# Optimization experiments

Hardware: AMD Instinct MI355X
Metric: run time of the kernel (lower is better)

## Reference

```python
import jax, jax.numpy as jnp
import numpy as np

R = 0.2          # stable-distribution hash bucket width
TABLE_SIZE = 2   # hash table size (buckets)
M = 5            # number of appended ALSH transform dims
EPS = 1e-12


def conv2d(x, W, b, pad):
    out = jax.lax.conv_general_dilated(
        x, W, window_strides=(1, 1), padding=[(pad, pad), (pad, pad)],
        dimension_numbers=('NCHW', 'OIHW', 'NCHW'))
    return out + b[None, :, None, None]


def maxpool2(x):
    return jax.lax.reduce_window(x, -jnp.inf, jax.lax.max,
                                 (1, 1, 2, 2), (1, 1, 2, 2), 'VALID')


def alsh_mask(x, W, a, c):
    """ALSH filter selection: hash P(kernels) and Q(query) with a stable
    distribution hash h(v)=floor((a.v+b)/r) mod table_size; active filters
    are those landing in the query's bucket. Returns [B, Cout] 0/1 mask.
    Multiplying conv output by this mask == gather active filters then
    zero_fill_missing back to full channel count."""
    Cout, Cin, kH, kW = W.shape
    Kf = W.reshape(Cout, -1)                       # [Cout, Cin*kH*kW]
    norms = jnp.linalg.norm(Kf, axis=1)
    Kn = Kf / (jnp.max(norms) + EPS)               # scale so all norms <= 1
    n = jnp.linalg.norm(Kn, axis=1, keepdims=True)
    # P transform: append norm^2, norm^4, ..., norm^(2^M)
    powers = jnp.concatenate([n ** (2 ** (i + 1)) for i in range(M)], axis=1)
    P = jnp.concatenate([Kn, powers], axis=1)      # [Cout, d+M]
    kh = jnp.mod(jnp.floor((P @ a + c[0]) / R), TABLE_SIZE)  # [Cout]
    # query vector: per-sample channel means broadcast over kernel support
    cm = x.mean(axis=(2, 3))                       # [B, Cin]
    q = jnp.repeat(cm, kH * kW, axis=1)            # [B, Cin*kH*kW] (cin,kh,kw order)
    qn = q / (jnp.linalg.norm(q, axis=1, keepdims=True) + EPS)
    # Q transform: append M halves
    Qv = jnp.concatenate([qn, jnp.full((q.shape[0], M), 0.5, q.dtype)], axis=1)
    qh = jnp.mod(jnp.floor((Qv @ a + c[0]) / R), TABLE_SIZE)  # [B]
    return (kh[None, :] == qh[:, None]).astype(x.dtype)       # [B, Cout]


def setup_inputs() -> dict:
    key = jax.random.key(0)
    ks = jax.random.split(key, 16)
    u = lambda k, s: jax.random.uniform(k, s, jnp.float32, 0.0, R)
    n = lambda k, s, sc=0.1: jax.random.normal(k, s, jnp.float32) * sc
    return {
        'x': jax.random.normal(ks[0], (4096, 3, 32, 32), jnp.float32),
        'W1': n(ks[1], (16, 3, 5, 5)), 'b1': n(ks[2], (16,)),
        'a1': jax.random.normal(ks[3], (80,), jnp.float32), 'c1': u(ks[4], (1,)),
        'W2': n(ks[5], (20, 16, 5, 5)), 'b2': n(ks[6], (20,)),
        'a2': jax.random.normal(ks[7], (405,), jnp.float32), 'c2': u(ks[8], (1,)),
        'W3': n(ks[9], (20, 20, 5, 5)), 'b3': n(ks[10], (20,)),
        'a3': jax.random.normal(ks[11], (505,), jnp.float32), 'c3': u(ks[12], (1,)),
        'Wo': n(ks[13], (10, 320)), 'bo': n(ks[14], (10,)),
    }


def reference(x, W1, b1, a1, c1, W2, b2, a2, c2, W3, b3, a3, c3, Wo, bo):
    m1 = alsh_mask(x, W1, a1, c1)
    h = jax.nn.relu(conv2d(x, W1, b1, 2)) * m1[:, :, None, None]
    h = maxpool2(h)                                # [B,16,16,16]
    m2 = alsh_mask(h, W2, a2, c2)
    h = jax.nn.relu(conv2d(h, W2, b2, 2)) * m2[:, :, None, None]
    h = maxpool2(h)                                # [B,20,8,8]
    m3 = alsh_mask(h, W3, a3, c3)
    h = jax.nn.relu(conv2d(h, W3, b3, 2)) * m3[:, :, None, None]
    # zero_fill_missing -> identity here: inactive channels already zero
    h = maxpool2(h)                                # [B,20,4,4]
    flat = h.reshape(h.shape[0], -1)               # [B,320]
    return flat @ Wo.T + bo
```

## Files before the change

### kernel.cpp

```cpp
#include <hip/hip_runtime.h>
#include <hip/hip_bf16.h>

#define EPSV 1e-12
#define RHASH 0.2

__device__ __forceinline__ int fmod2(double t) {
    return (int)(((long long)floor(t)) & 1LL);
}

__device__ __forceinline__ void load_row6(const float* base, float* r) {
    float2 a0 = *(const float2*)(base);
    float2 a1 = *(const float2*)(base + 2);
    float2 a2 = *(const float2*)(base + 4);
    r[0] = a0.x; r[1] = a0.y; r[2] = a1.x; r[3] = a1.y; r[4] = a2.x; r[5] = a2.y;
}

__device__ void layer_setup(const float* W, const float* a, double cval,
                            int Co, int Ci, int* kh, double* asum, double* qc,
                            double* s_norm, float* Wbuf, float* abuf)
{
    const int t = threadIdx.x;
    const int D = Ci * 25;
    for (int i = t; i < Co * D; i += 256) Wbuf[i] = W[i];
    for (int i = t; i < D + 5; i += 256) abuf[i] = a[i];
    __syncthreads();
    if (t < Co) {
        double s = 0;
        for (int j = 0; j < D; ++j) { double w = (double)Wbuf[t * D + j]; s += w * w; }
        s_norm[t] = sqrt(s);
    }
    __syncthreads();
    if (t == 0) {
        double mx = 0;
        for (int i = 0; i < Co; ++i) mx = fmax(mx, s_norm[i]);
        s_norm[23] = 1.0 / (mx + EPSV);
    }
    __syncthreads();
    double scale = s_norm[23];
    if (t < Co) {
        double dp = 0;
        for (int j = 0; j < D; ++j) dp += (double)Wbuf[t * D + j] * (double)abuf[j];
        dp *= scale;
        double n = s_norm[t] * scale;
        double p = n * n;
        for (int m = 0; m < 5; ++m) { dp += p * (double)abuf[D + m]; p *= p; }
        kh[t] = fmod2((dp + cval) / RHASH);
    }
    if (t >= 64 && t < 64 + Ci) {
        int c = t - 64;
        double s = 0;
        for (int j = 0; j < 25; ++j) s += (double)abuf[c * 25 + j];
        asum[c] = s;
    }
    if (t == 128) {
        double s = 0;
        for (int m = 0; m < 5; ++m) s += (double)abuf[D + m];
        *qc = 0.5 * s + cval;
    }
    __syncthreads();
}

__global__ __launch_bounds__(256) void setup_kernel(
    const float* W1, const float* a1, const float* c1,
    const float* W2, const float* a2, const float* c2,
    const float* W3, const float* a3, const float* c3,
    double* dmeta, int* imeta)
{
    __shared__ float Wbuf[10000];
    __shared__ float abuf[512];
    __shared__ double s_norm[24];
    layer_setup(W1, a1, (double)c1[0], 16, 3,  imeta + 0,  dmeta + 0,  dmeta + 39, s_norm, Wbuf, abuf);
    layer_setup(W2, a2, (double)c2[0], 20, 16, imeta + 16, dmeta + 3,  dmeta + 40, s_norm, Wbuf, abuf);
    layer_setup(W3, a3, (double)c3[0], 20, 20, imeta + 36, dmeta + 19, dmeta + 41, s_norm, Wbuf, abuf);
}

__global__ __launch_bounds__(256) void pack_kernel(const float* W1, const float* W2, const float* W3,
                                                   float* Wp1, float* Wp2, float* Wp3)
{
    int i = blockIdx.x * 256 + threadIdx.x;
    if (i < 1200) {
        int co = i & 15, r = i >> 4;
        int kx = r % 5, r2 = r / 5, ky = r2 % 5, ci = r2 / 5;
        Wp1[i] = W1[co * 75 + ci * 25 + ky * 5 + kx];
    } else if (i < 1200 + 8960) {
        int k = i - 1200;
        int j = k % 28, r = k / 28;
        int cog = r % 4, r2 = r / 4, ky = r2 % 5, ci = r2 / 5;
        Wp2[k] = (j < 25) ? W2[(cog * 5 + j / 5) * 400 + ci * 25 + ky * 5 + (j % 5)] : 0.f;
    } else if (i < 1200 + 8960 + 11200) {
        int k = i - 10160;
        int j = k % 28, r = k / 28;
        int cog = r % 4, r2 = r / 4, ky = r2 % 5, ci = r2 / 5;
        Wp3[k] = (j < 25) ? W3[(cog * 5 + j / 5) * 500 + ci * 25 + ky * 5 + (j % 5)] : 0.f;
    }
}

__global__ __launch_bounds__(256) void conv1_kernel(
    const float* __restrict__ x, const float* __restrict__ Wp1,
    const float* __restrict__ b1, const int* __restrict__ kh1,
    const double* __restrict__ dmeta, float* __restrict__ h1,
    int* __restrict__ qh2)
{
    __shared__ float xs[3][36][36];
    __shared__ float Ws[1200];
    __shared__ double s_red[3];
    __shared__ double s_ch[16][4];

    const int b = blockIdx.x, t = threadIdx.x;
    const int w = t >> 6, ln = t & 63;

    for (int i = t; i < 3 * 36 * 36; i += 256) (&xs[0][0][0])[i] = 0.f;
    for (int i = t; i < 600; i += 256) ((float2*)Ws)[i] = ((const float2*)Wp1)[i];
    __syncthreads();
    const float2* xb2 = (const float2*)(x + (size_t)b * 3072);
    for (int i = t; i < 1536; i += 256) {
        int idx = i * 2, c = idx >> 10, rem = idx & 1023;
        *(float2*)&xs[c][(rem >> 5) + 2][(rem & 31) + 2] = xb2[i];
    }
    __syncthreads();

    if (w < 3) {
        double s = 0;
        for (int j = 0; j < 16; ++j) {
            int i = ln + 64 * j;
            s += (double)xs[w][(i >> 5) + 2][(i & 31) + 2];
        }
        #pragma unroll
        for (int off = 32; off; off >>= 1) s += __shfl_xor(s, off);
        if (ln == 0) s_red[w] = s;
    }
    __syncthreads();
    double dp = 0, nn = 0;
    #pragma unroll
    for (int c = 0; c < 3; ++c) {
        double cm = s_red[c] * (1.0 / 1024.0);
        dp += cm * dmeta[c]; nn += cm * cm;
    }
    const int qh = fmod2((dp / (5.0 * sqrt(nn) + EPSV) + dmeta[39]) / RHASH);

    const int py = t >> 4, px = t & 15;
    const int y0 = 2 * py, x0 = 2 * px;

    float acc[16][4];
    #pragma unroll
    for (int c = 0; c < 16; ++c) {
        float bb = b1[c];
        acc[c][0] = bb; acc[c][1] = bb; acc[c][2] = bb; acc[c][3] = bb;
    }
    #pragma unroll
    for (int ci = 0; ci < 3; ++ci) {
        float cur[6], nxt[6];
        load_row6(&xs[ci][y0][x0], cur);
        load_row6(&xs[ci][y0 + 1][x0], nxt);
        #pragma unroll
        for (int ky = 0; ky < 5; ++ky) {
            const float* wbase = Ws + ((ci * 5 + ky) * 5) * 16;
            #pragma unroll
            for (int kx = 0; kx < 5; ++kx) {
                float wc[16];
                const float4* wp = (const float4*)(wbase + kx * 16);
                *(float4*)&wc[0]  = wp[0];
                *(float4*)&wc[4]  = wp[1];
                *(float4*)&wc[8]  = wp[2];
                *(float4*)&wc[12] = wp[3];
                #pragma unroll
                for (int c = 0; c < 16; ++c) {
                    acc[c][0] = fmaf(wc[c], cur[kx],     acc[c][0]);
                    acc[c][1] = fmaf(wc[c], cur[kx + 1], acc[c][1]);
                    acc[c][2] = fmaf(wc[c], nxt[kx],     acc[c][2]);
                    acc[c][3] = fmaf(wc[c], nxt[kx + 1], acc[c][3]);
                }
            }
            if (ky < 4) {
                #pragma unroll
                for (int j = 0; j < 6; ++j) cur[j] = nxt[j];
                load_row6(&xs[ci][y0 + ky + 2][x0], nxt);
            }
        }
    }

    float mv[16];
    float* hb = h1 + (size_t)b * 4096 + t;
    #pragma unroll
    for (int c = 0; c < 16; ++c) {
        float m = fmaxf(fmaxf(acc[c][0], acc[c][1]), fmaxf(acc[c][2], acc[c][3]));
        mv[c] = fmaxf(m, 0.f) * ((kh1[c] == qh) ? 1.f : 0.f);
        hb[c * 256] = mv[c];
    }
    #pragma unroll
    for (int c = 0; c < 16; ++c) {
        double s = (double)mv[c];
        #pragma unroll
        for (int off = 32; off; off >>= 1) s += __shfl_xor(s, off);
        if (ln == 0) s_ch[c][w] = s;
    }
    __syncthreads();
    if (t == 0) {
        double dp2 = 0, nn2 = 0;
        #pragma unroll
        for (int c = 0; c < 16; ++c) {
            double cm = (s_ch[c][0] + s_ch[c][1] + s_ch[c][2] + s_ch[c][3]) * (1.0 / 256.0);
            dp2 += cm * dmeta[3 + c]; nn2 += cm * cm;
        }
        qh2[b] = fmod2((dp2 / (5.0 * sqrt(nn2) + EPSV) + dmeta[40]) / RHASH);
    }
}

__global__ __launch_bounds__(256) void conv2_kernel(
    const float* __restrict__ h1, const float* __restrict__ Wp2,
    const float* __restrict__ b2, const int* __restrict__ kh2,
    const int* __restrict__ qh2, const double* __restrict__ dmeta,
    float* __restrict__ h2, int* __restrict__ qh3)
{
    __shared__ float xs[2][4][20][20];
    __shared__ float Ws[2240];
    __shared__ double s_ch[2][20];

    const int b0 = blockIdx.x * 2, t = threadIdx.x;
    const int cog = t >> 6, slot = t & 63;
    const int s = slot >> 5, py = (slot >> 2) & 7, pxp = slot & 3;
    const int y0 = 2 * py, x0a = 2 * pxp, x0b = 2 * pxp + 8;

    for (int i = t; i < 3200; i += 256) (&xs[0][0][0][0])[i] = 0.f;

    const int qh = qh2[b0 + s];
    float acc[5][8];
    #pragma unroll
    for (int c = 0; c < 5; ++c) {
        float bb = b2[cog * 5 + c];
        #pragma unroll
        for (int j = 0; j < 8; ++j) acc[c][j] = bb;
    }
    __syncthreads();

    for (int ch = 0; ch < 4; ++ch) {
        for (int i = t; i < 1120; i += 256)
            ((float2*)Ws)[i] = ((const float2*)(Wp2 + ch * 2240))[i];
        for (int i = t; i < 1024; i += 256) {
            int ss = i >> 9, r = i & 511, ci = r >> 7, rr = r & 127, p2 = rr * 2;
            *(float2*)&xs[ss][ci][(p2 >> 4) + 2][(p2 & 15) + 2] =
                ((const float2*)(h1 + (size_t)(b0 + ss) * 4096 + (ch * 4 + ci) * 256))[rr];
        }
        __syncthreads();

        #pragma unroll
        for (int ci = 0; ci < 4; ++ci) {
            float ca[6], na[6], cb[6], nb[6];
            load_row6(&xs[s][ci][y0][x0a], ca);
            load_row6(&xs[s][ci][y0 + 1][x0a], na);
            load_row6(&xs[s][ci][y0][x0b], cb);
            load_row6(&xs[s][ci][y0 + 1][x0b], nb);
            #pragma unroll
            for (int ky = 0; ky < 5; ++ky) {
                float wv[28];
                const float4* wp = (const float4*)&Ws[((ci * 5 + ky) * 4 + cog) * 28];
                *(float4*)&wv[0]  = wp[0];
                *(float4*)&wv[4]  = wp[1];
                *(float4*)&wv[8]  = wp[2];
                *(float4*)&wv[12] = wp[3];
                *(float4*)&wv[16] = wp[4];
                *(float4*)&wv[20] = wp[5];
                *(float4*)&wv[24] = wp[6];
                #pragma unroll
                for (int c = 0; c < 5; ++c) {
                    #pragma unroll
                    for (int kx = 0; kx < 5; ++kx) {
                        float wgt = wv[c * 5 + kx];
                        acc[c][0] = fmaf(wgt, ca[kx],     acc[c][0]);
                        acc[c][1] = fmaf(wgt, ca[kx + 1], acc[c][1]);
                        acc[c][2] = fmaf(wgt, na[kx],     acc[c][2]);
                        acc[c][3] = fmaf(wgt, na[kx + 1], acc[c][3]);
                        acc[c][4] = fmaf(wgt, cb[kx],     acc[c][4]);
                        acc[c][5] = fmaf(wgt, cb[kx + 1], acc[c][5]);
                        acc[c][6] = fmaf(wgt, nb[kx],     acc[c][6]);
                        acc[c][7] = fmaf(wgt, nb[kx + 1], acc[c][7]);
                    }
                }
                if (ky < 4) {
                    #pragma unroll
                    for (int j = 0; j < 6; ++j) { ca[j] = na[j]; cb[j] = nb[j]; }
                    load_row6(&xs[s][ci][y0 + ky + 2][x0a], na);
                    load_row6(&xs[s][ci][y0 + ky + 2][x0b], nb);
                }
            }
        }
        __syncthreads();
    }

    float* ob = h2 + (size_t)(b0 + s) * 1280 + py * 8 + pxp;
    double csum[5];
    #pragma unroll
    for (int c = 0; c < 5; ++c) {
        int co = cog * 5 + c;
        float mask = (kh2[co] == qh) ? 1.f : 0.f;
        float mA = fmaxf(fmaxf(acc[c][0], acc[c][1]), fmaxf(acc[c][2], acc[c][3]));
        float mB = fmaxf(fmaxf(acc[c][4], acc[c][5]), fmaxf(acc[c][6], acc[c][7]));
        float vA = fmaxf(mA, 0.f) * mask;
        float vB = fmaxf(mB, 0.f) * mask;
        ob[co * 64]     = vA;
        ob[co * 64 + 4] = vB;
        csum[c] = (double)vA + (double)vB;
    }
    #pragma unroll
    for (int c = 0; c < 5; ++c) {
        double sv = csum[c];
        #pragma unroll
        for (int off = 16; off; off >>= 1) sv += __shfl_xor(sv, off);
        if ((slot & 31) == 0) s_ch[s][cog * 5 + c] = sv;
    }
    __syncthreads();
    if (t < 2) {
        double dp2 = 0, nn2 = 0;
        #pragma unroll
        for (int c = 0; c < 20; ++c) {
            double cm = s_ch[t][c] * (1.0 / 64.0);
            dp2 += cm * dmeta[19 + c]; nn2 += cm * cm;
        }
        qh3[b0 + t] = fmod2((dp2 / (5.0 * sqrt(nn2) + EPSV) + dmeta[41]) / RHASH);
    }
}

__global__ __launch_bounds__(256) void conv3_kernel(
    const float* __restrict__ h2, const float* __restrict__ Wp3,
    const float* __restrict__ b3, const int* __restrict__ kh3,
    const int* __restrict__ qh3,
    const float* __restrict__ Wo, const float* __restrict__ bo,
    float* __restrict__ out, int B)
{
    __shared__ float xs[4][5][12][12];
    __shared__ float Ws[2800];
    __shared__ float flat[4][320];

    const int b0 = blockIdx.x * 4, t = threadIdx.x;
    const int s = t >> 6, q = t & 63, cog = q >> 4, pos = q & 15;
    const int py = pos >> 2, px = pos & 3;
    const int y0 = 2 * py, x0 = 2 * px;
    const int b = b0 + s;

    for (int i = t; i < 4 * 5 * 144; i += 256) (&xs[0][0][0][0])[i] = 0.f;

    const int qh = (b < B) ? qh3[b] : 0;
    float acc[5][4];
    #pragma unroll
    for (int c = 0; c < 5; ++c) {
        float bb = b3[cog * 5 + c];
        acc[c][0] = bb; acc[c][1] = bb; acc[c][2] = bb; acc[c][3] = bb;
    }
    __syncthreads();

    for (int ch = 0; ch < 4; ++ch) {
        for (int i = t; i < 1400; i += 256)
            ((float2*)Ws)[i] = ((const float2*)(Wp3 + ch * 2800))[i];
        for (int i = t; i < 640; i += 256) {
            int ss = i / 160, r = i - ss * 160, ci = r >> 5, rr = r & 31, p2 = rr * 2;
            if (b0 + ss < B)
                *(float2*)&xs[ss][ci][(p2 >> 3) + 2][(p2 & 7) + 2] =
                    ((const float2*)(h2 + (size_t)(b0 + ss) * 1280 + (ch * 5 + ci) * 64))[rr];
        }
        __syncthreads();

        #pragma unroll
        for (int ci = 0; ci < 5; ++ci) {
            float cur[6], nxt[6];
            load_row6(&xs[s][ci][y0][x0], cur);
            load_row6(&xs[s][ci][y0 + 1][x0], nxt);
            #pragma unroll
            for (int ky = 0; ky < 5; ++ky) {
                float wv[28];
                const float4* wp = (const float4*)&Ws[((ci * 5 + ky) * 4 + cog) * 28];
                *(float4*)&wv[0]  = wp[0];
                *(float4*)&wv[4]  = wp[1];
                *(float4*)&wv[8]  = wp[2];
                *(float4*)&wv[12] = wp[3];
                *(float4*)&wv[16] = wp[4];
                *(float4*)&wv[20] = wp[5];
                *(float4*)&wv[24] = wp[6];
                #pragma unroll
                for (int c = 0; c < 5; ++c) {
                    #pragma unroll
                    for (int kx = 0; kx < 5; ++kx) {
                        float wgt = wv[c * 5 + kx];
                        acc[c][0] = fmaf(wgt, cur[kx],     acc[c][0]);
                        acc[c][1] = fmaf(wgt, cur[kx + 1], acc[c][1]);
                        acc[c][2] = fmaf(wgt, nxt[kx],     acc[c][2]);
                        acc[c][3] = fmaf(wgt, nxt[kx + 1], acc[c][3]);
                    }
                }
                if (ky < 4) {
                    #pragma unroll
                    for (int j = 0; j < 6; ++j) cur[j] = nxt[j];
                    load_row6(&xs[s][ci][y0 + ky + 2][x0], nxt);
                }
            }
        }
        __syncthreads();
    }

    #pragma unroll
    for (int c = 0; c < 5; ++c) {
        int co = cog * 5 + c;
        float m = fmaxf(fmaxf(acc[c][0], acc[c][1]), fmaxf(acc[c][2], acc[c][3]));
        flat[s][co * 16 + pos] = fmaxf(m, 0.f) * ((kh3[co] == qh) ? 1.f : 0.f);
    }
    __syncthreads();

    if (t < 160) {
        const int g = t >> 2, qq = t & 3;
        const int ss = g / 10, o = g - ss * 10;
        float a = 0.f;
        const float* wr = Wo + o * 320;
        for (int k = qq; k < 320; k += 4) a = fmaf(flat[ss][k], wr[k], a);
        a += __shfl_xor(a, 1);
        a += __shfl_xor(a, 2);
        if (qq == 0 && b0 + ss < B) out[(size_t)(b0 + ss) * 10 + o] = a + bo[o];
    }
}

extern "C" void kernel_launch(void* const* d_in, const int* in_sizes, int n_in,
                              void* d_out, int out_size, void* d_ws, size_t ws_size,
                              hipStream_t stream)
{
    const float* x  = (const float*)d_in[0];
    const float* W1 = (const float*)d_in[1];
    const float* b1 = (const float*)d_in[2];
    const float* a1 = (const float*)d_in[3];
    const float* c1 = (const float*)d_in[4];
    const float* W2 = (const float*)d_in[5];
    const float* b2 = (const float*)d_in[6];
    const float* a2 = (const float*)d_in[7];
    const float* c2 = (const float*)d_in[8];
    const float* W3 = (const float*)d_in[9];
    const float* b3 = (const float*)d_in[10];
    const float* a3 = (const float*)d_in[11];
    const float* c3 = (const float*)d_in[12];
    const float* Wo = (const float*)d_in[13];
    const float* bo = (const float*)d_in[14];
    float* out = (float*)d_out;

    const int B = in_sizes[0] / 3072;

    float* h1  = (float*)d_ws;
    float* h2  = h1 + (size_t)B * 4096;
    float* Wp1 = h2 + (size_t)B * 1280;
    float* Wp2 = Wp1 + 1200;
    float* Wp3 = Wp2 + 8960;
    double* dmeta = (double*)(Wp3 + 11200);
    int* imeta = (int*)(dmeta + 42);
    int* qh2 = imeta + 56;
    int* qh3 = qh2 + B;

    setup_kernel<<<1, 256, 0, stream>>>(W1, a1, c1, W2, a2, c2, W3, a3, c3, dmeta, imeta);
    pack_kernel<<<84, 256, 0, stream>>>(W1, W2, W3, Wp1, Wp2, Wp3);
    conv1_kernel<<<B, 256, 0, stream>>>(x, Wp1, b1, imeta, dmeta, h1, qh2);
    conv2_kernel<<<B / 2, 256, 0, stream>>>(h1, Wp2, b2, imeta + 16, qh2, dmeta, h2, qh3);
    conv3_kernel<<<(B + 3) / 4, 256, 0, stream>>>(h2, Wp3, b3, imeta + 36, qh3, Wo, bo, out, B);
}
```

Before: 572.8 us.

## Re-tile conv1 to 8 channels by 8 outputs and stream weights in conv2/conv3

Conv1 now splits the 16 output channels across two thread halves, with each thread computing 8 channels for two pooled positions (8 accumulators each) instead of 16 channels for one position. This reduces the per-thread accumulator and weight register footprint, and the cross-wave channel reduction is adjusted to match. Conv2 and conv3 no longer stage a 28-float weight array in registers; they consume float4 LDS loads directly through FMA macros. All conv kernels add a launch-bounds minimum of 4 blocks to push for higher occupancy, which risks register spills.

```diff
diff --git a/kernel.cpp b/kernel.cpp
--- a/kernel.cpp
+++ b/kernel.cpp
@@ -14,6 +14,16 @@
     float2 a2 = *(const float2*)(base + 4);
     r[0] = a0.x; r[1] = a0.y; r[2] = a1.x; r[3] = a1.y; r[4] = a2.x; r[5] = a2.y;
 }
+
+#define FMA8(c,kx,w) { float wg=(w); \
+  acc[c][0]=fmaf(wg,ca[kx],acc[c][0]); acc[c][1]=fmaf(wg,ca[(kx)+1],acc[c][1]); \
+  acc[c][2]=fmaf(wg,na[kx],acc[c][2]); acc[c][3]=fmaf(wg,na[(kx)+1],acc[c][3]); \
+  acc[c][4]=fmaf(wg,cb[kx],acc[c][4]); acc[c][5]=fmaf(wg,cb[(kx)+1],acc[c][5]); \
+  acc[c][6]=fmaf(wg,nb[kx],acc[c][6]); acc[c][7]=fmaf(wg,nb[(kx)+1],acc[c][7]); }
+
+#define FMA4(c,kx,w) { float wg=(w); \
+  acc[c][0]=fmaf(wg,cur[kx],acc[c][0]); acc[c][1]=fmaf(wg,cur[(kx)+1],acc[c][1]); \
+  acc[c][2]=fmaf(wg,nxt[kx],acc[c][2]); acc[c][3]=fmaf(wg,nxt[(kx)+1],acc[c][3]); }
 
 __device__ void layer_setup(const float* W, const float* a, double cval,
                             int Co, int Ci, int* kh, double* asum, double* qc,
@@ -95,7 +105,7 @@
     }
 }
 
-__global__ __launch_bounds__(256) void conv1_kernel(
+__global__ __launch_bounds__(256, 4) void conv1_kernel(
     const float* __restrict__ x, const float* __restrict__ Wp1,
     const float* __restrict__ b1, const int* __restrict__ kh1,
     const double* __restrict__ dmeta, float* __restrict__ h1,
@@ -104,7 +114,7 @@
     __shared__ float xs[3][36][36];
     __shared__ float Ws[1200];
     __shared__ double s_red[3];
-    __shared__ double s_ch[16][4];
+    __shared__ double s_ch[16][2];
 
     const int b = blockIdx.x, t = threadIdx.x;
     const int w = t >> 6, ln = t & 63;
@@ -138,75 +148,72 @@
     }
     const int qh = fmod2((dp / (5.0 * sqrt(nn) + EPSV) + dmeta[39]) / RHASH);
 
-    const int py = t >> 4, px = t & 15;
-    const int y0 = 2 * py, x0 = 2 * px;
-
-    float acc[16][4];
-    #pragma unroll
-    for (int c = 0; c < 16; ++c) {
-        float bb = b1[c];
-        acc[c][0] = bb; acc[c][1] = bb; acc[c][2] = bb; acc[c][3] = bb;
-    }
+    const int cog = t >> 7, r7 = t & 127;
+    const int py = r7 >> 3, pxp = r7 & 7;
+    const int y0 = 2 * py, x0a = 2 * pxp, x0b = 2 * pxp + 16;
+
+    float acc[8][8];
+    #pragma unroll
+    for (int c = 0; c < 8; ++c) {
+        float bb = b1[cog * 8 + c];
+        #pragma unroll
+        for (int j = 0; j < 8; ++j) acc[c][j] = bb;
+    }
+
     #pragma unroll
     for (int ci = 0; ci < 3; ++ci) {
-        float cur[6], nxt[6];
-        load_row6(&xs[ci][y0][x0], cur);
-        load_row6(&xs[ci][y0 + 1][x0], nxt);
         #pragma unroll
         for (int ky = 0; ky < 5; ++ky) {
-            const float* wbase = Ws + ((ci * 5 + ky) * 5) * 16;
+            float ca[6], na[6], cb[6], nb[6];
+            load_row6(&xs[ci][y0 + ky][x0a],     ca);
+            load_row6(&xs[ci][y0 + ky + 1][x0a], na);
+            load_row6(&xs[ci][y0 + ky][x0b],     cb);
+            load_row6(&xs[ci][y0 + ky + 1][x0b], nb);
+            const float4* wq = (const float4*)&Ws[((ci * 5 + ky) * 5) * 16 + cog * 8];
             #pragma unroll
             for (int kx = 0; kx < 5; ++kx) {
-                float wc[16];
-                const float4* wp = (const float4*)(wbase + kx * 16);
-                *(float4*)&wc[0]  = wp[0];
-                *(float4*)&wc[4]  = wp[1];
-                *(float4*)&wc[8]  = wp[2];
-                *(float4*)&wc[12] = wp[3];
-                #pragma unroll
-                for (int c = 0; c < 16; ++c) {
-                    acc[c][0] = fmaf(wc[c], cur[kx],     acc[c][0]);
-                    acc[c][1] = fmaf(wc[c], cur[kx + 1], acc[c][1]);
-                    acc[c][2] = fmaf(wc[c], nxt[kx],     acc[c][2]);
-                    acc[c][3] = fmaf(wc[c], nxt[kx + 1], acc[c][3]);
-                }
+                float4 w0 = wq[kx * 4];
+                float4 w1 = wq[kx * 4 + 1];
+                FMA8(0, kx, w0.x) FMA8(1, kx, w0.y) FMA8(2, kx, w0.z) FMA8(3, kx, w0.w)
+                FMA8(4, kx, w1.x) FMA8(5, kx, w1.y) FMA8(6, kx, w1.z) FMA8(7, kx, w1.w)
             }
-            if (ky < 4) {
-                #pragma unroll
-                for (int j = 0; j < 6; ++j) cur[j] = nxt[j];
-                load_row6(&xs[ci][y0 + ky + 2][x0], nxt);
-            }
-        }
-    }
-
-    float mv[16];
-    float* hb = h1 + (size_t)b * 4096 + t;
-    #pragma unroll
-    for (int c = 0; c < 16; ++c) {
-        float m = fmaxf(fmaxf(acc[c][0], acc[c][1]), fmaxf(acc[c][2], acc[c][3]));
-        mv[c] = fmaxf(m, 0.f) * ((kh1[c] == qh) ? 1.f : 0.f);
-        hb[c * 256] = mv[c];
-    }
-    #pragma unroll
-    for (int c = 0; c < 16; ++c) {
-        double s = (double)mv[c];
+        }
+    }
+
+    float* hb = h1 + (size_t)b * 4096 + py * 16 + pxp;
+    double csum[8];
+    #pragma unroll
+    for (int c = 0; c < 8; ++c) {
+        int co = cog * 8 + c;
+        float mask = (kh1[co] == qh) ? 1.f : 0.f;
+        float mA = fmaxf(fmaxf(acc[c][0], acc[c][1]), fmaxf(acc[c][2], acc[c][3]));
+        float mB = fmaxf(fmaxf(acc[c][4], acc[c][5]), fmaxf(acc[c][6], acc[c][7]));
+        float vA = fmaxf(mA, 0.f) * mask;
+        float vB = fmaxf(mB, 0.f) * mask;
+        hb[co * 256]     = vA;
+        hb[co * 256 + 8] = vB;
+        csum[c] = (double)vA + (double)vB;
+    }
+    #pragma unroll
+    for (int c = 0; c < 8; ++c) {
+        double s = csum[c];
         #pragma unroll
         for (int off = 32; off; off >>= 1) s += __shfl_xor(s, off);
-        if (ln == 0) s_ch[c][w] = s;
+        if (ln == 0) s_ch[cog * 8 + c][w & 1] = s;
     }
     __syncthreads();
     if (t == 0) {
         double dp2 = 0, nn2 = 0;
         #pragma unroll
         for (int c = 0; c < 16; ++c) {
-            double cm = (s_ch[c][0] + s_ch[c][1] + s_ch[c][2] + s_ch[c][3]) * (1.0 / 256.0);
+            double cm = (s_ch[c][0] + s_ch[c][1]) * (1.0 / 256.0);
             dp2 += cm * dmeta[3 + c]; nn2 += cm * cm;
         }
         qh2[b] = fmod2((dp2 / (5.0 * sqrt(nn2) + EPSV) + dmeta[40]) / RHASH);
     }
 }
 
-__global__ __launch_bounds__(256) void conv2_kernel(
+__global__ __launch_bounds__(256, 4) void conv2_kernel(
     const float* __restrict__ h1, const float* __restrict__ Wp2,
     const float* __restrict__ b2, const int* __restrict__ kh2,
     const int* __restrict__ qh2, const double* __restrict__ dmeta,
@@ -252,30 +259,16 @@
             load_row6(&xs[s][ci][y0 + 1][x0b], nb);
             #pragma unroll
             for (int ky = 0; ky < 5; ++ky) {
-                float wv[28];
-                const float4* wp = (const float4*)&Ws[((ci * 5 + ky) * 4 + cog) * 28];
-                *(float4*)&wv[0]  = wp[0];
-                *(float4*)&wv[4]  = wp[1];
-                *(float4*)&wv[8]  = wp[2];
-                *(float4*)&wv[12] = wp[3];
-                *(float4*)&wv[16] = wp[4];
-                *(float4*)&wv[20] = wp[5];
-                *(float4*)&wv[24] = wp[6];
-                #pragma unroll
-                for (int c = 0; c < 5; ++c) {
-                    #pragma unroll
-                    for (int kx = 0; kx < 5; ++kx) {
-                        float wgt = wv[c * 5 + kx];
-                        acc[c][0] = fmaf(wgt, ca[kx],     acc[c][0]);
-                        acc[c][1] = fmaf(wgt, ca[kx + 1], acc[c][1]);
-                        acc[c][2] = fmaf(wgt, na[kx],     acc[c][2]);
-                        acc[c][3] = fmaf(wgt, na[kx + 1], acc[c][3]);
-                        acc[c][4] = fmaf(wgt, cb[kx],     acc[c][4]);
-                        acc[c][5] = fmaf(wgt, cb[kx + 1], acc[c][5]);
-                        acc[c][6] = fmaf(wgt, nb[kx],     acc[c][6]);
-                        acc[c][7] = fmaf(wgt, nb[kx + 1], acc[c][7]);
-                    }
-                }
+                const float* wrow = &Ws[((ci * 5 + ky) * 4 + cog) * 28];
+                const float4* wq = (const float4*)wrow;
+                float4 q;
+                q = wq[0]; FMA8(0, 0, q.x) FMA8(0, 1, q.y) FMA8(0, 2, q.z) FMA8(0, 3, q.w)
+                q = wq[1]; FMA8(0, 4, q.x) FMA8(1, 0, q.y) FMA8(1, 1, q.z) FMA8(1, 2, q.w)
+                q = wq[2]; FMA8(1, 3, q.x) FMA8(1, 4, q.y) FMA8(2, 0, q.z) FMA8(2, 1, q.w)
+                q = wq[3]; FMA8(2, 2, q.x) FMA8(2, 3, q.y) FMA8(2, 4, q.z) FMA8(3, 0, q.w)
+                q = wq[4]; FMA8(3, 1, q.x) FMA8(3, 2, q.y) FMA8(3, 3, q.z) FMA8(3, 4, q.w)
+                q = wq[5]; FMA8(4, 0, q.x) FMA8(4, 1, q.y) FMA8(4, 2, q.z) FMA8(4, 3, q.w)
+                FMA8(4, 4, wrow[24])
                 if (ky < 4) {
                     #pragma unroll
                     for (int j = 0; j < 6; ++j) { ca[j] = na[j]; cb[j] = nb[j]; }
@@ -320,7 +313,7 @@
     }
 }
 
-__global__ __launch_bounds__(256) void conv3_kernel(
+__global__ __launch_bounds__(256, 4) void conv3_kernel(
     const float* __restrict__ h2, const float* __restrict__ Wp3,
     const float* __restrict__ b3, const int* __restrict__ kh3,
     const int* __restrict__ qh3,
@@ -332,7 +325,7 @@
     __shared__ float flat[4][320];
 
     const int b0 = blockIdx.x * 4, t = threadIdx.x;
-    const int s = t >> 6, q = t & 63, cog = q >> 4, pos = q & 15;
+    const int s = t >> 6, q0 = t & 63, cog = q0 >> 4, pos = q0 & 15;
     const int py = pos >> 2, px = pos & 3;
     const int y0 = 2 * py, x0 = 2 * px;
     const int b = b0 + s;
@@ -366,26 +359,16 @@
             load_row6(&xs[s][ci][y0 + 1][x0], nxt);
             #pragma unroll
             for (int ky = 0; ky < 5; ++ky) {
-                float wv[28];
-                const float4* wp = (const float4*)&Ws[((ci * 5 + ky) * 4 + cog) * 28];
-                *(float4*)&wv[0]  = wp[0];
-                *(float4*)&wv[4]  = wp[1];
-                *(float4*)&wv[8]  = wp[2];
-                *(float4*)&wv[12] = wp[3];
-                *(float4*)&wv[16] = wp[4];
-                *(float4*)&wv[20] = wp[5];
-                *(float4*)&wv[24] = wp[6];
-                #pragma unroll
-                for (int c = 0; c < 5; ++c) {
-                    #pragma unroll
-                    for (int kx = 0; kx < 5; ++kx) {
-                        float wgt = wv[c * 5 + kx];
-                        acc[c][0] = fmaf(wgt, cur[kx],     acc[c][0]);
-                        acc[c][1] = fmaf(wgt, cur[kx + 1], acc[c][1]);
-                        acc[c][2] = fmaf(wgt, nxt[kx],     acc[c][2]);
-                        acc[c][3] = fmaf(wgt, nxt[kx + 1], acc[c][3]);
-                    }
-                }
+                const float* wrow = &Ws[((ci * 5 + ky) * 4 + cog) * 28];
+                const float4* wq = (const float4*)wrow;
+                float4 q;
+                q = wq[0]; FMA4(0, 0, q.x) FMA4(0, 1, q.y) FMA4(0, 2, q.z) FMA4(0, 3, q.w)
+                q = wq[1]; FMA4(0, 4, q.x) FMA4(1, 0, q.y) FMA4(1, 1, q.z) FMA4(1, 2, q.w)
+                q = wq[2]; FMA4(1, 3, q.x) FMA4(1, 4, q.y) FMA4(2, 0, q.z) FMA4(2, 1, q.w)
+                q = wq[3]; FMA4(2, 2, q.x) FMA4(2, 3, q.y) FMA4(2, 4, q.z) FMA4(3, 0, q.w)
+                q = wq[4]; FMA4(3, 1, q.x) FMA4(3, 2, q.y) FMA4(3, 3, q.z) FMA4(3, 4, q.w)
+                q = wq[5]; FMA4(4, 0, q.x) FMA4(4, 1, q.y) FMA4(4, 2, q.z) FMA4(4, 3, q.w)
+                FMA4(4, 4, wrow[24])
                 if (ky < 4) {
                     #pragma unroll
                     for (int j = 0; j < 6; ++j) cur[j] = nxt[j];
```

New measurement: 570.2 us. Within noise of the previous version (-0.5%).
